# Performance work log

Hardware: AMD Instinct MI355X
Metric: run time of the kernel (lower is better)

Reference implementation:

```python
import jax, jax.numpy as jnp
import numpy as np

N = 100000   # nodes
E = 1600000  # edges
C = 128      # in_channels
H = 128      # hidden_channels


def _gcn_conv(x, row, col, w, W, b, n_nodes):
    """PyG-style GCNConv: x' = D^{-1/2}(A+I)D^{-1/2} (x W) + b, with edge weights."""
    x = x @ W  # [N, out]
    # add self-loops with weight 1
    loop = jnp.arange(n_nodes, dtype=row.dtype)
    row2 = jnp.concatenate([row, loop])
    col2 = jnp.concatenate([col, loop])
    w2 = jnp.concatenate([w, jnp.ones((n_nodes,), dtype=w.dtype)])
    # symmetric normalization: deg over destination (col), per PyG gcn_norm
    deg = jax.ops.segment_sum(w2, col2, num_segments=n_nodes)
    dinv = jnp.where(deg > 0, jax.lax.rsqrt(jnp.where(deg > 0, deg, 1.0)), 0.0)
    norm = dinv[row2] * w2 * dinv[col2]  # [E+N]
    # message = norm * x[src]; aggregate (scatter-add) into dst
    msg = norm[:, None] * x[row2]  # [E+N, out]
    out = jax.ops.segment_sum(msg, col2, num_segments=n_nodes)
    return out + b


def setup_inputs() -> dict:
    key = jax.random.key(0)
    k0, k1, k2, k3, k4 = jax.random.split(key, 5)
    node_feature = jax.random.normal(k0, (N, C), dtype=jnp.float32)
    edge_index = jax.random.randint(k1, (2, E), 0, N, dtype=jnp.int32)
    edge_weight = jax.random.uniform(k2, (E,), dtype=jnp.float32)
    W1 = jax.random.normal(k3, (C, H), dtype=jnp.float32) * (1.0 / np.sqrt(C))
    b1 = jnp.zeros((H,), dtype=jnp.float32)
    W2 = jax.random.normal(k4, (H, 1), dtype=jnp.float32) * (1.0 / np.sqrt(H))
    b2 = jnp.zeros((1,), dtype=jnp.float32)
    return {"node_feature": node_feature, "edge_index": edge_index,
            "edge_weight": edge_weight, "W1": W1, "b1": b1, "W2": W2, "b2": b2}


def reference(node_feature, edge_index, edge_weight, W1, b1, W2, b2):
    row, col = edge_index[0], edge_index[1]
    h = _gcn_conv(node_feature, row, col, edge_weight, W1, b1, N)
    out = _gcn_conv(h, row, col, edge_weight, W2, b2, N)  # [N, 1]
    return out
```

## Files before the change

kernel.cpp:

```cpp
#include <hip/hip_runtime.h>

#define CH 128
#define CHUNK 8192
#define BSH 8
#define BNODES 256
#define MAXB 512
#define PNT 512
#define AGG_NT 1024
#define GEMV_BLOCKS 1024

__global__ __launch_bounds__(256) void k_uw_hist(const float* __restrict__ W1,
                                                 const float* __restrict__ b1,
                                                 const float* __restrict__ W2,
                                                 float* __restrict__ u,
                                                 const int* __restrict__ col,
                                                 int* __restrict__ Ht,
                                                 int nbuck, int nchunk, int e_cnt) {
    __shared__ int h[MAXB];
    int b = blockIdx.x, tid = threadIdx.x;
    if (b == nchunk) {
        int wv = tid >> 6, lane = tid & 63;
        float2 vv = *(const float2*)(W2 + lane * 2);
        for (int r = wv; r <= CH; r += 4) {
            const float* rowp = (r < CH) ? (W1 + (size_t)r * CH) : b1;
            float2 xv = *(const float2*)(rowp + lane * 2);
            float acc = xv.x * vv.x + xv.y * vv.y;
#pragma unroll
            for (int m = 32; m; m >>= 1) acc += __shfl_xor(acc, m);
            if (lane == 0) u[r] = acc;
        }
        return;
    }
    for (int k = tid; k < nbuck; k += 256) h[k] = 0;
    __syncthreads();
    int e0 = b * CHUNK, e1 = min(e0 + CHUNK, e_cnt);
    for (int e = e0 + tid; e < e1; e += 256)
        atomicAdd(&h[col[e] >> BSH], 1);
    __syncthreads();
    for (int k = tid; k < nbuck; k += 256) Ht[(size_t)b * nbuck + k] = h[k];
}

__global__ __launch_bounds__(256) void k_gemv_colscan(const float* __restrict__ X,
                                                      const float* __restrict__ u,
                                                      float* __restrict__ t,
                                                      const int* __restrict__ Ht,
                                                      int* __restrict__ Hs,
                                                      int* __restrict__ coltot,
                                                      int n, int nchunk, int nbuck,
                                                      int nbCols) {
    int b = blockIdx.x, tid = threadIdx.x;
    if (b < nbCols) {
        int j = b * 4 + (tid >> 6);
        if (j >= nbuck) return;
        int lane = tid & 63;
        int run = 0;
        for (int base = 0; base < nchunk; base += 64) {
            int idx = base + lane;
            int v = (idx < nchunk) ? Ht[(size_t)idx * nbuck + j] : 0;
            int incl = v;
#pragma unroll
            for (int d = 1; d < 64; d <<= 1) {
                int up = __shfl_up(incl, d);
                if (lane >= d) incl += up;
            }
            if (idx < nchunk) Hs[(size_t)idx * nbuck + j] = run + incl - v;
            run += __shfl(incl, 63);
        }
        if (lane == 0) coltot[j] = run;
        return;
    }
    int gb = b - nbCols;
    int hw = gb * 8 + (tid >> 5);
    int l  = tid & 31;
    float4 uv = *(const float4*)(u + l * 4);
    const int stride = GEMV_BLOCKS * 8;
    for (int base = hw; base < n; base += stride * 4) {
        int r0 = base, r1 = base + stride, r2 = base + 2 * stride, r3 = base + 3 * stride;
        float a0 = 0.f, a1 = 0.f, a2 = 0.f, a3 = 0.f;
        if (r0 < n) { float4 x = *(const float4*)(X + (size_t)r0 * CH + l * 4);
                      a0 = x.x * uv.x + x.y * uv.y + x.z * uv.z + x.w * uv.w; }
        if (r1 < n) { float4 x = *(const float4*)(X + (size_t)r1 * CH + l * 4);
                      a1 = x.x * uv.x + x.y * uv.y + x.z * uv.z + x.w * uv.w; }
        if (r2 < n) { float4 x = *(const float4*)(X + (size_t)r2 * CH + l * 4);
                      a2 = x.x * uv.x + x.y * uv.y + x.z * uv.z + x.w * uv.w; }
        if (r3 < n) { float4 x = *(const float4*)(X + (size_t)r3 * CH + l * 4);
                      a3 = x.x * uv.x + x.y * uv.y + x.z * uv.z + x.w * uv.w; }
#pragma unroll
        for (int m = 16; m; m >>= 1) {
            a0 += __shfl_xor(a0, m); a1 += __shfl_xor(a1, m);
            a2 += __shfl_xor(a2, m); a3 += __shfl_xor(a3, m);
        }
        if (l == 0) {
            if (r0 < n) t[r0] = a0;
            if (r1 < n) t[r1] = a1;
            if (r2 < n) t[r2] = a2;
            if (r3 < n) t[r3] = a3;
        }
    }
}

__global__ __launch_bounds__(PNT) void k_permute(const int* __restrict__ row,
                                                 const int* __restrict__ col,
                                                 const float* __restrict__ w,
                                                 const int* __restrict__ Hs,
                                                 const int* __restrict__ coltot,
                                                 int* __restrict__ bstart,
                                                 int2* __restrict__ ep,
                                                 int nbuck, int e_cnt) {
    __shared__ int bs[MAXB + 1];
    __shared__ int cur[MAXB];
    int b = blockIdx.x, tid = threadIdx.x;
    if (tid < 64) {
        int run = 0;
        for (int base = 0; base < nbuck; base += 64) {
            int idx = base + tid;
            int v = (idx < nbuck) ? coltot[idx] : 0;
            int incl = v;
#pragma unroll
            for (int d = 1; d < 64; d <<= 1) {
                int up = __shfl_up(incl, d);
                if (tid >= d) incl += up;
            }
            if (idx < nbuck) bs[idx] = run + incl - v;
            run += __shfl(incl, 63);
        }
        if (tid == 0) bs[nbuck] = run;
    }
    __syncthreads();
    for (int k = tid; k < nbuck; k += PNT)
        cur[k] = bs[k] + Hs[(size_t)b * nbuck + k];
    __syncthreads();
    int e0 = b * CHUNK, e1 = min(e0 + CHUNK, e_cnt);
    for (int e = e0 + tid; e < e1; e += PNT) {
        int r = row[e], c = col[e];
        float wv = w[e];
        int pos = atomicAdd(&cur[c >> BSH], 1);
        ep[pos] = make_int2(r | ((c & (BNODES - 1)) << 17), __float_as_int(wv));
    }
    if (b == 0)
        for (int k = tid; k <= nbuck; k += PNT) bstart[k] = bs[k];
}

__global__ __launch_bounds__(AGG_NT) void k_adeg(const int2* __restrict__ ep,
                                                 const int* __restrict__ bstart,
                                                 const float* __restrict__ t,
                                                 float* __restrict__ dinv,
                                                 float* __restrict__ p, int n) {
    __shared__ float acc[BNODES];
    int b = blockIdx.x, tid = threadIdx.x;
    if (tid < BNODES) acc[tid] = 0.f;
    __syncthreads();
    int j1 = bstart[b + 1];
    for (int j = bstart[b] + tid; j < j1; j += AGG_NT) {
        int2 kv = ep[j];
        atomicAdd(&acc[kv.x >> 17], __int_as_float(kv.y));
    }
    __syncthreads();
    int node = (b << BSH) + tid;
    if (tid < BNODES && node < n) {
        float di = rsqrtf(1.0f + acc[tid]);
        dinv[node] = di;
        p[node] = di * t[node];
    }
}

__global__ __launch_bounds__(AGG_NT) void k_as1(const int2* __restrict__ ep,
                                                const int* __restrict__ bstart,
                                                const float* __restrict__ p,
                                                const float* __restrict__ dinv,
                                                const float* __restrict__ u,
                                                float* __restrict__ q, int n) {
    __shared__ float acc[BNODES];
    int b = blockIdx.x, tid = threadIdx.x;
    if (tid < BNODES) acc[tid] = 0.f;
    __syncthreads();
    int j1 = bstart[b + 1];
    for (int j = bstart[b] + tid; j < j1; j += AGG_NT) {
        int2 kv = ep[j];
        atomicAdd(&acc[kv.x >> 17], __int_as_float(kv.y) * p[kv.x & 0x1FFFF]);
    }
    __syncthreads();
    int node = (b << BSH) + tid;
    if (tid < BNODES && node < n) {
        float di = dinv[node];
        float s1 = di * (p[node] + acc[tid]);
        q[node] = di * (s1 + u[CH]);
    }
}

__global__ __launch_bounds__(AGG_NT) void k_aout(const int2* __restrict__ ep,
                                                 const int* __restrict__ bstart,
                                                 const float* __restrict__ q,
                                                 const float* __restrict__ dinv,
                                                 const float* __restrict__ b2,
                                                 float* __restrict__ out, int n) {
    __shared__ float acc[BNODES];
    int b = blockIdx.x, tid = threadIdx.x;
    if (tid < BNODES) acc[tid] = 0.f;
    __syncthreads();
    int j1 = bstart[b + 1];
    for (int j = bstart[b] + tid; j < j1; j += AGG_NT) {
        int2 kv = ep[j];
        atomicAdd(&acc[kv.x >> 17], __int_as_float(kv.y) * q[kv.x & 0x1FFFF]);
    }
    __syncthreads();
    int node = (b << BSH) + tid;
    if (tid < BNODES && node < n)
        out[node] = b2[0] + dinv[node] * (q[node] + acc[tid]);
}

extern "C" void kernel_launch(void* const* d_in, const int* in_sizes, int n_in,
                              void* d_out, int out_size, void* d_ws, size_t ws_size,
                              hipStream_t stream) {
    const float* x   = (const float*)d_in[0];
    const int*   ei  = (const int*)d_in[1];
    const float* w   = (const float*)d_in[2];
    const float* W1  = (const float*)d_in[3];
    const float* b1  = (const float*)d_in[4];
    const float* W2  = (const float*)d_in[5];
    const float* b2  = (const float*)d_in[6];
    float* out = (float*)d_out;

    const int n     = in_sizes[0] / CH;
    const int e_cnt = in_sizes[2];
    const int* row = ei;
    const int* col = ei + e_cnt;

    const int nbuck  = (n + BNODES - 1) >> BSH;
    const int nchunk = (e_cnt + CHUNK - 1) / CHUNK;
    const int nbCols = (nbuck + 3) / 4;

    int2*  ep     = (int2*)d_ws;
    float* u      = (float*)(ep + e_cnt);
    float* t      = u + 132;
    float* dinv   = t + n;
    float* p      = dinv + n;
    float* q      = p + n;
    int*   coltot = (int*)(q + n);
    int*   bstart = coltot + nbuck;
    int*   Ht     = bstart + nbuck + 1;
    int*   Hs     = Ht + (size_t)nchunk * nbuck;

    k_uw_hist<<<nchunk + 1, 256, 0, stream>>>(W1, b1, W2, u, col, Ht,
                                              nbuck, nchunk, e_cnt);
    k_gemv_colscan<<<nbCols + GEMV_BLOCKS, 256, 0, stream>>>(x, u, t, Ht, Hs, coltot,
                                                             n, nchunk, nbuck, nbCols);
    k_permute<<<nchunk, PNT, 0, stream>>>(row, col, w, Hs, coltot, bstart, ep,
                                          nbuck, e_cnt);
    k_adeg<<<nbuck, AGG_NT, 0, stream>>>(ep, bstart, t, dinv, p, n);
    k_as1<<<nbuck, AGG_NT, 0, stream>>>(ep, bstart, p, dinv, u, q, n);
    k_aout<<<nbuck, AGG_NT, 0, stream>>>(ep, bstart, q, dinv, b2, out, n);
}
```

Baseline: 181.3 us.

## Fuse column scan into permute kernel and shrink node buckets to 128

Removes the separate column-scan pass. Each permute block now recomputes its own per-bucket prefix and totals by walking the histogram over all chunks, and the GEMV is merged into the same launch. Buckets shrink to 128 nodes, doubling the bucket count, and the aggregation kernels move to 256 threads per block. This saves a kernel launch and the Hs/coltot round trip, at the cost of redundant histogram reads in every permute block (nchunk x nbuck per block).

```diff
diff --git a/kernel.cpp b/kernel.cpp
--- a/kernel.cpp
+++ b/kernel.cpp
@@ -2,20 +2,20 @@
 
 #define CH 128
 #define CHUNK 8192
-#define BSH 8
-#define BNODES 256
-#define MAXB 512
+#define BSH 7
+#define BNODES 128
+#define MAXB 800
 #define PNT 512
-#define AGG_NT 1024
-#define GEMV_BLOCKS 1024
-
-__global__ __launch_bounds__(256) void k_uw_hist(const float* __restrict__ W1,
-                                                 const float* __restrict__ b1,
-                                                 const float* __restrict__ W2,
-                                                 float* __restrict__ u,
-                                                 const int* __restrict__ col,
-                                                 int* __restrict__ Ht,
-                                                 int nbuck, int nchunk, int e_cnt) {
+#define ANT 256
+#define GEMV_BLOCKS 512
+
+__global__ __launch_bounds__(256) void k_head(const float* __restrict__ W1,
+                                              const float* __restrict__ b1,
+                                              const float* __restrict__ W2,
+                                              float* __restrict__ u,
+                                              const int* __restrict__ col,
+                                              int* __restrict__ Ht,
+                                              int nbuck, int nchunk, int e_cnt) {
     __shared__ int h[MAXB];
     int b = blockIdx.x, tid = threadIdx.x;
     if (b == nchunk) {
@@ -40,81 +40,70 @@
     for (int k = tid; k < nbuck; k += 256) Ht[(size_t)b * nbuck + k] = h[k];
 }
 
-__global__ __launch_bounds__(256) void k_gemv_colscan(const float* __restrict__ X,
-                                                      const float* __restrict__ u,
-                                                      float* __restrict__ t,
-                                                      const int* __restrict__ Ht,
-                                                      int* __restrict__ Hs,
-                                                      int* __restrict__ coltot,
-                                                      int n, int nchunk, int nbuck,
-                                                      int nbCols) {
-    int b = blockIdx.x, tid = threadIdx.x;
-    if (b < nbCols) {
-        int j = b * 4 + (tid >> 6);
-        if (j >= nbuck) return;
-        int lane = tid & 63;
-        int run = 0;
-        for (int base = 0; base < nchunk; base += 64) {
-            int idx = base + lane;
-            int v = (idx < nchunk) ? Ht[(size_t)idx * nbuck + j] : 0;
-            int incl = v;
+__global__ __launch_bounds__(PNT) void k_mid(const float* __restrict__ X,
+                                             const float* __restrict__ u,
+                                             float* __restrict__ t,
+                                             const int* __restrict__ row,
+                                             const int* __restrict__ col,
+                                             const float* __restrict__ w,
+                                             const int* __restrict__ Ht,
+                                             int* __restrict__ bstart,
+                                             int2* __restrict__ ep,
+                                             int n, int nbuck, int nchunk,
+                                             int nPerm, int e_cnt) {
+    __shared__ int ct[MAXB];
+    __shared__ int pre[MAXB];
+    __shared__ int bs[MAXB + 1];
+    int b = blockIdx.x, tid = threadIdx.x;
+
+    if (b >= nPerm) {
+        int gb = b - nPerm;
+        int hw = gb * (PNT / 32) + (tid >> 5);
+        int l  = tid & 31;
+        float4 uv = *(const float4*)(u + l * 4);
+        const int stride = GEMV_BLOCKS * (PNT / 32);
+        for (int base = hw; base < n; base += stride * 4) {
+            int r0 = base, r1 = base + stride, r2 = base + 2 * stride, r3 = base + 3 * stride;
+            float a0 = 0.f, a1 = 0.f, a2 = 0.f, a3 = 0.f;
+            if (r0 < n) { float4 x = *(const float4*)(X + (size_t)r0 * CH + l * 4);
+                          a0 = x.x * uv.x + x.y * uv.y + x.z * uv.z + x.w * uv.w; }
+            if (r1 < n) { float4 x = *(const float4*)(X + (size_t)r1 * CH + l * 4);
+                          a1 = x.x * uv.x + x.y * uv.y + x.z * uv.z + x.w * uv.w; }
+            if (r2 < n) { float4 x = *(const float4*)(X + (size_t)r2 * CH + l * 4);
+                          a2 = x.x * uv.x + x.y * uv.y + x.z * uv.z + x.w * uv.w; }
+            if (r3 < n) { float4 x = *(const float4*)(X + (size_t)r3 * CH + l * 4);
+                          a3 = x.x * uv.x + x.y * uv.y + x.z * uv.z + x.w * uv.w; }
 #pragma unroll
-            for (int d = 1; d < 64; d <<= 1) {
-                int up = __shfl_up(incl, d);
-                if (lane >= d) incl += up;
+            for (int m = 16; m; m >>= 1) {
+                a0 += __shfl_xor(a0, m); a1 += __shfl_xor(a1, m);
+                a2 += __shfl_xor(a2, m); a3 += __shfl_xor(a3, m);
             }
-            if (idx < nchunk) Hs[(size_t)idx * nbuck + j] = run + incl - v;
-            run += __shfl(incl, 63);
-        }
-        if (lane == 0) coltot[j] = run;
+            if (l == 0) {
+                if (r0 < n) t[r0] = a0;
+                if (r1 < n) t[r1] = a1;
+                if (r2 < n) t[r2] = a2;
+                if (r3 < n) t[r3] = a3;
+            }
+        }
         return;
     }
-    int gb = b - nbCols;
-    int hw = gb * 8 + (tid >> 5);
-    int l  = tid & 31;
-    float4 uv = *(const float4*)(u + l * 4);
-    const int stride = GEMV_BLOCKS * 8;
-    for (int base = hw; base < n; base += stride * 4) {
-        int r0 = base, r1 = base + stride, r2 = base + 2 * stride, r3 = base + 3 * stride;
-        float a0 = 0.f, a1 = 0.f, a2 = 0.f, a3 = 0.f;
-        if (r0 < n) { float4 x = *(const float4*)(X + (size_t)r0 * CH + l * 4);
-                      a0 = x.x * uv.x + x.y * uv.y + x.z * uv.z + x.w * uv.w; }
-        if (r1 < n) { float4 x = *(const float4*)(X + (size_t)r1 * CH + l * 4);
-                      a1 = x.x * uv.x + x.y * uv.y + x.z * uv.z + x.w * uv.w; }
-        if (r2 < n) { float4 x = *(const float4*)(X + (size_t)r2 * CH + l * 4);
-                      a2 = x.x * uv.x + x.y * uv.y + x.z * uv.z + x.w * uv.w; }
-        if (r3 < n) { float4 x = *(const float4*)(X + (size_t)r3 * CH + l * 4);
-                      a3 = x.x * uv.x + x.y * uv.y + x.z * uv.z + x.w * uv.w; }
-#pragma unroll
-        for (int m = 16; m; m >>= 1) {
-            a0 += __shfl_xor(a0, m); a1 += __shfl_xor(a1, m);
-            a2 += __shfl_xor(a2, m); a3 += __shfl_xor(a3, m);
-        }
-        if (l == 0) {
-            if (r0 < n) t[r0] = a0;
-            if (r1 < n) t[r1] = a1;
-            if (r2 < n) t[r2] = a2;
-            if (r3 < n) t[r3] = a3;
-        }
-    }
-}
-
-__global__ __launch_bounds__(PNT) void k_permute(const int* __restrict__ row,
-                                                 const int* __restrict__ col,
-                                                 const float* __restrict__ w,
-                                                 const int* __restrict__ Hs,
-                                                 const int* __restrict__ coltot,
-                                                 int* __restrict__ bstart,
-                                                 int2* __restrict__ ep,
-                                                 int nbuck, int e_cnt) {
-    __shared__ int bs[MAXB + 1];
-    __shared__ int cur[MAXB];
-    int b = blockIdx.x, tid = threadIdx.x;
+
+    for (int j = tid; j < nbuck; j += PNT) {
+        int run = 0, pr = 0;
+        for (int c = 0; c < nchunk; ++c) {
+            int v = Ht[(size_t)c * nbuck + j];
+            if (c < b) pr += v;
+            run += v;
+        }
+        ct[j] = run;
+        pre[j] = pr;
+    }
+    __syncthreads();
     if (tid < 64) {
         int run = 0;
         for (int base = 0; base < nbuck; base += 64) {
             int idx = base + tid;
-            int v = (idx < nbuck) ? coltot[idx] : 0;
+            int v = (idx < nbuck) ? ct[idx] : 0;
             int incl = v;
 #pragma unroll
             for (int d = 1; d < 64; d <<= 1) {
@@ -127,31 +116,30 @@
         if (tid == 0) bs[nbuck] = run;
     }
     __syncthreads();
-    for (int k = tid; k < nbuck; k += PNT)
-        cur[k] = bs[k] + Hs[(size_t)b * nbuck + k];
+    for (int j = tid; j < nbuck; j += PNT) pre[j] += bs[j];
     __syncthreads();
     int e0 = b * CHUNK, e1 = min(e0 + CHUNK, e_cnt);
     for (int e = e0 + tid; e < e1; e += PNT) {
         int r = row[e], c = col[e];
         float wv = w[e];
-        int pos = atomicAdd(&cur[c >> BSH], 1);
+        int pos = atomicAdd(&pre[c >> BSH], 1);
         ep[pos] = make_int2(r | ((c & (BNODES - 1)) << 17), __float_as_int(wv));
     }
     if (b == 0)
         for (int k = tid; k <= nbuck; k += PNT) bstart[k] = bs[k];
 }
 
-__global__ __launch_bounds__(AGG_NT) void k_adeg(const int2* __restrict__ ep,
-                                                 const int* __restrict__ bstart,
-                                                 const float* __restrict__ t,
-                                                 float* __restrict__ dinv,
-                                                 float* __restrict__ p, int n) {
+__global__ __launch_bounds__(ANT) void k_adeg(const int2* __restrict__ ep,
+                                              const int* __restrict__ bstart,
+                                              const float* __restrict__ t,
+                                              float* __restrict__ dinv,
+                                              float* __restrict__ p, int n) {
     __shared__ float acc[BNODES];
     int b = blockIdx.x, tid = threadIdx.x;
     if (tid < BNODES) acc[tid] = 0.f;
     __syncthreads();
     int j1 = bstart[b + 1];
-    for (int j = bstart[b] + tid; j < j1; j += AGG_NT) {
+    for (int j = bstart[b] + tid; j < j1; j += ANT) {
         int2 kv = ep[j];
         atomicAdd(&acc[kv.x >> 17], __int_as_float(kv.y));
     }
@@ -164,18 +152,18 @@
     }
 }
 
-__global__ __launch_bounds__(AGG_NT) void k_as1(const int2* __restrict__ ep,
-                                                const int* __restrict__ bstart,
-                                                const float* __restrict__ p,
-                                                const float* __restrict__ dinv,
-                                                const float* __restrict__ u,
-                                                float* __restrict__ q, int n) {
+__global__ __launch_bounds__(ANT) void k_as1(const int2* __restrict__ ep,
+                                             const int* __restrict__ bstart,
+                                             const float* __restrict__ p,
+                                             const float* __restrict__ dinv,
+                                             const float* __restrict__ u,
+                                             float* __restrict__ q, int n) {
     __shared__ float acc[BNODES];
     int b = blockIdx.x, tid = threadIdx.x;
     if (tid < BNODES) acc[tid] = 0.f;
     __syncthreads();
     int j1 = bstart[b + 1];
-    for (int j = bstart[b] + tid; j < j1; j += AGG_NT) {
+    for (int j = bstart[b] + tid; j < j1; j += ANT) {
         int2 kv = ep[j];
         atomicAdd(&acc[kv.x >> 17], __int_as_float(kv.y) * p[kv.x & 0x1FFFF]);
     }
@@ -188,18 +176,18 @@
     }
 }
 
-__global__ __launch_bounds__(AGG_NT) void k_aout(const int2* __restrict__ ep,
-                                                 const int* __restrict__ bstart,
-                                                 const float* __restrict__ q,
-                                                 const float* __restrict__ dinv,
-                                                 const float* __restrict__ b2,
-                                                 float* __restrict__ out, int n) {
+__global__ __launch_bounds__(ANT) void k_aout(const int2* __restrict__ ep,
+                                              const int* __restrict__ bstart,
+                                              const float* __restrict__ q,
+                                              const float* __restrict__ dinv,
+                                              const float* __restrict__ b2,
+                                              float* __restrict__ out, int n) {
     __shared__ float acc[BNODES];
     int b = blockIdx.x, tid = threadIdx.x;
     if (tid < BNODES) acc[tid] = 0.f;
     __syncthreads();
     int j1 = bstart[b + 1];
-    for (int j = bstart[b] + tid; j < j1; j += AGG_NT) {
+    for (int j = bstart[b] + tid; j < j1; j += ANT) {
         int2 kv = ep[j];
         atomicAdd(&acc[kv.x >> 17], __int_as_float(kv.y) * q[kv.x & 0x1FFFF]);
     }
@@ -228,7 +216,6 @@
 
     const int nbuck  = (n + BNODES - 1) >> BSH;
     const int nchunk = (e_cnt + CHUNK - 1) / CHUNK;
-    const int nbCols = (nbuck + 3) / 4;
 
     int2*  ep     = (int2*)d_ws;
     float* u      = (float*)(ep + e_cnt);
@@ -236,18 +223,15 @@
     float* dinv   = t + n;
     float* p      = dinv + n;
     float* q      = p + n;
-    int*   coltot = (int*)(q + n);
-    int*   bstart = coltot + nbuck;
+    int*   bstart = (int*)(q + n);
     int*   Ht     = bstart + nbuck + 1;
-    int*   Hs     = Ht + (size_t)nchunk * nbuck;
-
-    k_uw_hist<<<nchunk + 1, 256, 0, stream>>>(W1, b1, W2, u, col, Ht,
-                                              nbuck, nchunk, e_cnt);
-    k_gemv_colscan<<<nbCols + GEMV_BLOCKS, 256, 0, stream>>>(x, u, t, Ht, Hs, coltot,
-                                                             n, nchunk, nbuck, nbCols);
-    k_permute<<<nchunk, PNT, 0, stream>>>(row, col, w, Hs, coltot, bstart, ep,
-                                          nbuck, e_cnt);
-    k_adeg<<<nbuck, AGG_NT, 0, stream>>>(ep, bstart, t, dinv, p, n);
-    k_as1<<<nbuck, AGG_NT, 0, stream>>>(ep, bstart, p, dinv, u, q, n);
-    k_aout<<<nbuck, AGG_NT, 0, stream>>>(ep, bstart, q, dinv, b2, out, n);
-}
+
+    k_head<<<nchunk + 1, 256, 0, stream>>>(W1, b1, W2, u, col, Ht,
+                                           nbuck, nchunk, e_cnt);
+    k_mid<<<nchunk + GEMV_BLOCKS, PNT, 0, stream>>>(x, u, t, row, col, w, Ht,
+                                                    bstart, ep, n, nbuck, nchunk,
+                                                    nchunk, e_cnt);
+    k_adeg<<<nbuck, ANT, 0, stream>>>(ep, bstart, t, dinv, p, n);
+    k_as1<<<nbuck, ANT, 0, stream>>>(ep, bstart, p, dinv, u, q, n);
+    k_aout<<<nbuck, ANT, 0, stream>>>(ep, bstart, q, dinv, b2, out, n);
+}
```

After: 274.9 us. +51.6%, slower.
